# Kernel tuning notes

Measured on AMD Instinct MI355X. Metric: run time of the kernel, lower is better.

Reference implementation:

```python
import jax, jax.numpy as jnp
import numpy as np

N_HEAD = 16
LN_EPS = 1e-5


def _rope_tables(T, hd, dtype):
    # Standard GPT-NeoX style rotary tables: cos/sin of shape [T, hd]
    inv = 1.0 / (10000.0 ** (np.arange(0, hd, 2, dtype=np.float64) / hd))
    freqs = np.outer(np.arange(T), inv)
    emb = np.concatenate([freqs, freqs], axis=-1)
    return jnp.asarray(np.cos(emb), dtype), jnp.asarray(np.sin(emb), dtype)


def _rotate_half(x):
    x1, x2 = jnp.split(x, 2, axis=-1)
    return jnp.concatenate([-x2, x1], axis=-1)


def _layernorm(x, g, b):
    mu = x.mean(-1, keepdims=True)
    var = x.var(-1, keepdims=True)
    return (x - mu) / jnp.sqrt(var + LN_EPS) * g + b


def _heads(x, H):
    B, T, C = x.shape
    return x.reshape(B, T, H, C // H).transpose(0, 2, 1, 3)  # [B,H,T,hd]


def _lin_attention(Q, K, V, causal):
    # Q,K,V: [B,H,T,hd]; ELU+1 feature map, RoPE on features, denom = sum_s Q.K
    Qf = jax.nn.elu(Q) + 1.0
    Kf = jax.nn.elu(K) + 1.0
    hd = Qf.shape[-1]
    cq, sq = _rope_tables(Qf.shape[2], hd, Qf.dtype)
    ck, sk = _rope_tables(Kf.shape[2], hd, Kf.dtype)
    Qr = Qf * cq + _rotate_half(Qf) * sq
    Kr = Kf * ck + _rotate_half(Kf) * sk
    # denom.sum(-1) == Qf . (sum_s Kf) -- avoid materializing a second TxS matrix
    denom = jnp.einsum('bhtd,bhd->bht', Qf, Kf.sum(axis=2))[..., None]
    att = jnp.einsum('bhtd,bhsd->bhts', Qr, Kr)
    if causal:
        T, S = att.shape[-2], att.shape[-1]
        att = jnp.where(jnp.tril(jnp.ones((T, S), dtype=bool)), att, 0.0)
    att = att / denom
    y = jnp.einsum('bhts,bhsd->bhtd', att, V)
    B, H, T, hd = y.shape
    return y.transpose(0, 2, 1, 3).reshape(B, T, H * hd)


def _forward(x, memory, ln1_g, ln1_b, sa_qkv_w, sa_qkv_b, sa_proj_w, sa_proj_b,
             ln2_g, ln2_b, ca_q_w, ca_q_b, ca_kv_w, ca_kv_b, ca_proj_w, ca_proj_b,
             ln3_g, ln3_b, fc_w, fc_b, fcp_w, fcp_b):
    H = N_HEAD
    # causal self-attention
    h = _layernorm(x, ln1_g, ln1_b)
    qkv = h @ sa_qkv_w + sa_qkv_b
    Q, K, V = jnp.split(qkv, 3, axis=-1)
    y = _lin_attention(_heads(Q, H), _heads(K, H), _heads(V, H), causal=True)
    x = x + (y @ sa_proj_w + sa_proj_b)
    # cross-attention
    h = _layernorm(x, ln2_g, ln2_b)
    q = h @ ca_q_w + ca_q_b
    kv = memory @ ca_kv_w + ca_kv_b
    K, V = jnp.split(kv, 2, axis=-1)
    y = _lin_attention(_heads(q, H), _heads(K, H), _heads(V, H), causal=False)
    x = x + (y @ ca_proj_w + ca_proj_b)
    # MLP with tanh-approx GELU
    h = _layernorm(x, ln3_g, ln3_b)
    h = jax.nn.gelu(h @ fc_w + fc_b, approximate=True)
    x = x + (h @ fcp_w + fcp_b)
    return x


def setup_inputs() -> dict:
    key = jax.random.key(0)
    ks = jax.random.split(key, 12)
    B, T, S, C = 2, 1024, 1024, 1024
    w = lambda k, shape: jax.random.normal(k, shape, dtype=jnp.float32) * 0.02
    return {
        'x': jax.random.normal(ks[0], (B, T, C), dtype=jnp.float32),
        'memory': jax.random.normal(ks[1], (B, S, C), dtype=jnp.float32),
        'ln1_g': jnp.ones((C,), jnp.float32), 'ln1_b': jnp.zeros((C,), jnp.float32),
        'sa_qkv_w': w(ks[2], (C, 3 * C)), 'sa_qkv_b': jnp.zeros((3 * C,), jnp.float32),
        'sa_proj_w': w(ks[3], (C, C)), 'sa_proj_b': jnp.zeros((C,), jnp.float32),
        'ln2_g': jnp.ones((C,), jnp.float32), 'ln2_b': jnp.zeros((C,), jnp.float32),
        'ca_q_w': w(ks[4], (C, C)), 'ca_q_b': jnp.zeros((C,), jnp.float32),
        'ca_kv_w': w(ks[5], (C, 2 * C)), 'ca_kv_b': jnp.zeros((2 * C,), jnp.float32),
        'ca_proj_w': w(ks[6], (C, C)), 'ca_proj_b': jnp.zeros((C,), jnp.float32),
        'ln3_g': jnp.ones((C,), jnp.float32), 'ln3_b': jnp.zeros((C,), jnp.float32),
        'fc_w': w(ks[7], (C, 4 * C)), 'fc_b': jnp.zeros((4 * C,), jnp.float32),
        'fcp_w': w(ks[8], (4 * C, C)), 'fcp_b': jnp.zeros((C,), jnp.float32),
    }


def reference(x, memory, ln1_g, ln1_b, sa_qkv_w, sa_qkv_b, sa_proj_w, sa_proj_b,
              ln2_g, ln2_b, ca_q_w, ca_q_b, ca_kv_w, ca_kv_b, ca_proj_w, ca_proj_b,
              ln3_g, ln3_b, fc_w, fc_b, fcp_w, fcp_b):
    return _forward(x, memory, ln1_g, ln1_b, sa_qkv_w, sa_qkv_b, sa_proj_w, sa_proj_b,
                    ln2_g, ln2_b, ca_q_w, ca_q_b, ca_kv_w, ca_kv_b, ca_proj_w, ca_proj_b,
                    ln3_g, ln3_b, fc_w, fc_b, fcp_w, fcp_b)
```

## Files before the change

kernel.cpp:

```cpp
#include <hip/hip_runtime.h>
#include <math.h>

#define BB 2
#define TT 1024
#define CC 1024
#define HH 16
#define HD 64
#define MM (BB*TT)

typedef unsigned short u16;
typedef unsigned int u32;
typedef short s16x8 __attribute__((ext_vector_type(8)));
typedef float f32x4 __attribute__((ext_vector_type(4)));

__device__ __forceinline__ u16 f2bf(float f) {
    u32 u = __builtin_bit_cast(u32, f);
    u += 0x7fffu + ((u >> 16) & 1u);
    return (u16)(u >> 16);
}
__device__ __forceinline__ float bf2f(u16 h) {
    return __builtin_bit_cast(float, ((u32)h) << 16);
}
__device__ __forceinline__ void gload16(const void* g, void* l) {
    __builtin_amdgcn_global_load_lds((const __attribute__((address_space(1))) u32*)g,
                                     (__attribute__((address_space(3))) u32*)l, 16, 0, 0);
}
__device__ __forceinline__ float gelu_tanh(float x) {
    float x3 = x * x * x;
    return 0.5f * x * (1.0f + tanhf(0.7978845608028654f * (x + 0.044715f * x3)));
}
__device__ __forceinline__ float elu1(float v) {
    return (v > 0.0f) ? v + 1.0f : expf(v);
}

__device__ __forceinline__ void wtile(const float* __restrict__ in, u16* __restrict__ out,
                                      int K, int N, int local, float (*tl)[65]) {
    int tilesX = N >> 6;
    int n0 = (local % tilesX) * 64, k0 = (local / tilesX) * 64;
    int c = threadIdx.x & 63, r4 = threadIdx.x >> 6;
    #pragma unroll
    for (int i = 0; i < 16; ++i) {
        int r = r4 * 16 + i;
        tl[r][c] = in[(size_t)(k0 + r) * N + n0 + c];
    }
    __syncthreads();
    #pragma unroll
    for (int i = 0; i < 16; ++i) {
        int r = r4 * 16 + i;
        out[(size_t)(n0 + r) * K + k0 + c] = f2bf(tl[c][r]);
    }
}

__global__ __launch_bounds__(256) void prep_kernel(
        const float* __restrict__ w_qkv, u16* __restrict__ t_qkv,
        const float* __restrict__ w_pr,  u16* __restrict__ t_pr,
        const float* __restrict__ w_caq, u16* __restrict__ t_caq,
        const float* __restrict__ w_cakv,u16* __restrict__ t_cakv,
        const float* __restrict__ w_capr,u16* __restrict__ t_capr,
        const float* __restrict__ w_fc,  u16* __restrict__ t_fc,
        const float* __restrict__ w_fcp, u16* __restrict__ t_fcp,
        const float* __restrict__ memF,  u16* __restrict__ memB,
        float* __restrict__ cosT, float* __restrict__ sinT,
        const float* __restrict__ x, const float* __restrict__ ln1_g,
        const float* __restrict__ ln1_b, u16* __restrict__ hB) {
    __shared__ float tl[64][65];
    int bid = blockIdx.x;
    if (bid < 768)        wtile(w_qkv,  t_qkv,  1024, 3072, bid, tl);
    else if (bid < 1024)  wtile(w_pr,   t_pr,   1024, 1024, bid - 768, tl);
    else if (bid < 1280)  wtile(w_caq,  t_caq,  1024, 1024, bid - 1024, tl);
    else if (bid < 1792)  wtile(w_cakv, t_cakv, 1024, 2048, bid - 1280, tl);
    else if (bid < 2048)  wtile(w_capr, t_capr, 1024, 1024, bid - 1792, tl);
    else if (bid < 3072)  wtile(w_fc,   t_fc,   1024, 4096, bid - 2048, tl);
    else if (bid < 4096)  wtile(w_fcp,  t_fcp,  4096, 1024, bid - 3072, tl);
    else if (bid < 6144) {
        int i = (bid - 4096) * 256 + threadIdx.x;
        float4 v = reinterpret_cast<const float4*>(memF)[i];
        uint2 p;
        p.x = (u32)f2bf(v.x) | ((u32)f2bf(v.y) << 16);
        p.y = (u32)f2bf(v.z) | ((u32)f2bf(v.w) << 16);
        reinterpret_cast<uint2*>(memB)[i] = p;
    } else if (bid < 6272) {
        int idx = (bid - 6144) * 256 + threadIdx.x;
        int t = idx >> 5, d = idx & 31;
        double inv = pow(10000.0, -((double)d) / 32.0);
        double ang = (double)t * inv;
        cosT[t * 32 + d] = (float)cos(ang);
        sinT[t * 32 + d] = (float)sin(ang);
    } else {
        int row = bid - 6272;
        float4 v = reinterpret_cast<const float4*>(x + (size_t)row * CC)[threadIdx.x];
        float s  = v.x + v.y + v.z + v.w;
        float sq = v.x*v.x + v.y*v.y + v.z*v.z + v.w*v.w;
        #pragma unroll
        for (int off = 32; off >= 1; off >>= 1) {
            s  += __shfl_down(s, off);
            sq += __shfl_down(sq, off);
        }
        __shared__ float ls[4], lsq[4];
        int wave = threadIdx.x >> 6, lane = threadIdx.x & 63;
        if (lane == 0) { ls[wave] = s; lsq[wave] = sq; }
        __syncthreads();
        s  = ls[0] + ls[1] + ls[2] + ls[3];
        sq = lsq[0] + lsq[1] + lsq[2] + lsq[3];
        float mean = s * (1.0f / CC);
        float var  = sq * (1.0f / CC) - mean * mean;
        float rstd = rsqrtf(var + 1e-5f);
        float4 gv = reinterpret_cast<const float4*>(ln1_g)[threadIdx.x];
        float4 bv = reinterpret_cast<const float4*>(ln1_b)[threadIdx.x];
        float o0 = (v.x - mean) * rstd * gv.x + bv.x;
        float o1 = (v.y - mean) * rstd * gv.y + bv.y;
        float o2 = (v.z - mean) * rstd * gv.z + bv.z;
        float o3 = (v.w - mean) * rstd * gv.w + bv.w;
        uint2 p;
        p.x = (u32)f2bf(o0) | ((u32)f2bf(o1) << 16);
        p.y = (u32)f2bf(o2) | ((u32)f2bf(o3) << 16);
        reinterpret_cast<uint2*>(hB + (size_t)row * CC)[threadIdx.x] = p;
    }
}

#define M_F32RES 0
#define M_GELU   1
#define M_QKV    2
#define M_PART   5
#define M_CAQKV  6

template <int MODE>
__device__ __forceinline__ void emit(int row, int col, float v,
                                     const float* __restrict__ res,
                                     float* __restrict__ oF, u16* __restrict__ o1,
                                     u16* __restrict__ o2, u16* __restrict__ o3, int N) {
    if constexpr (MODE == M_F32RES) {
        size_t o = (size_t)row * N + col;
        oF[o] = v + res[o];
    } else if constexpr (MODE == M_GELU) {
        o1[(size_t)row * N + col] = f2bf(gelu_tanh(v));
    } else {
        int b = row >> 10, t = row & 1023;
        if (col < 1024) {
            int h = col >> 6, d = col & 63;
            o1[(((size_t)(b * HH + h)) * TT + t) * HD + d] = f2bf(elu1(v));
        } else if (col < 2048) {
            int c = col - 1024, h = c >> 6, d = c & 63;
            o2[(((size_t)(b * HH + h)) * TT + t) * HD + d] = f2bf(elu1(v));
        } else {
            int c = col - 2048, h = c >> 6, d = c & 63;
            o3[(((size_t)(b * HH + h)) * HD + d) * TT + t] = f2bf(v);
        }
    }
}

template <int BM, int BN, int MODE, int SPLITK>
__global__ __launch_bounds__(512, 8) void gemm_bf16(const u16* __restrict__ A,
                                                    const u16* __restrict__ A2,
                                                    const u16* __restrict__ BT,
                                                    const u16* __restrict__ BT2,
                                                    const float* __restrict__ bias,
                                                    const float* __restrict__ bias2,
                                                    const float* __restrict__ res,
                                                    float* __restrict__ oF,
                                                    u16* __restrict__ o1,
                                                    u16* __restrict__ o2,
                                                    u16* __restrict__ o3,
                                                    float* __restrict__ ksumP,
                                                    int N, int K) {
    constexpr int WM = BM / 4, WN = BN / 2;
    constexpr int FI = WM / 16, FJ = WN / 16;
    constexpr int IA = BM * 8 / 512;
    constexpr int IB = BN * 8 / 512;
    __shared__ u16 As[BM * 64];
    __shared__ u16 Bs[BN * 64];
    int tid = threadIdx.x;
    int wave = tid >> 6, lane = tid & 63;
    int wr = wave >> 1, wc = wave & 1;
    int gx = gridDim.x, gy = gridDim.y;
    int lid = blockIdx.x + gx * blockIdx.y;
    int chunk = (gx * gy) >> 3;
    int swz = (lid & 7) * chunk + (lid >> 3);
    int bx = swz % gx, by = swz / gx;
    int row0 = by * BM, col0 = bx * BN;
    const u16* Ause = A;
    const u16* Buse = BT;
    const float* buse = bias;
    if constexpr (MODE == M_CAQKV) {
        if (col0 >= 1024) {
            Ause = A2;
            Buse = BT2 - (size_t)1024 * K;
            buse = bias2 - 1024;
        }
    }
    int kbeg = 0, kcnt = K;
    if constexpr (SPLITK > 1) { kcnt = K / SPLITK; kbeg = blockIdx.z * kcnt; }
    int kend = kbeg + kcnt;

    f32x4 acc[FI][FJ] = {};
    int lr = lane & 15;
    for (int kt = kbeg; kt < kend; kt += 64) {
        __syncthreads();
        #pragma unroll
        for (int i = 0; i < IA; ++i) {
            int s = tid + i * 512;
            int r = s >> 3, kb = s & 7;
            int kbs = kb ^ (r & 7);
            gload16(Ause + (size_t)(row0 + r) * K + kt + kbs * 8, &As[s * 8]);
        }
        #pragma unroll
        for (int i = 0; i < IB; ++i) {
            int s = tid + i * 512;
            int r = s >> 3, kb = s & 7;
            int kbs = kb ^ (r & 7);
            gload16(Buse + (size_t)(col0 + r) * K + kt + kbs * 8, &Bs[s * 8]);
        }
        __syncthreads();
        #pragma unroll
        for (int ks = 0; ks < 2; ++ks) {
            s16x8 a[FI], b[FJ];
            int kc = ks * 4 + (lane >> 4);
            int sw = (kc ^ (lr & 7)) * 8;
            #pragma unroll
            for (int i = 0; i < FI; ++i)
                a[i] = *reinterpret_cast<const s16x8*>(&As[(wr * WM + i * 16 + lr) * 64 + sw]);
            #pragma unroll
            for (int j = 0; j < FJ; ++j)
                b[j] = *reinterpret_cast<const s16x8*>(&Bs[(wc * WN + j * 16 + lr) * 64 + sw]);
            __builtin_amdgcn_s_setprio(1);
            #pragma unroll
            for (int i = 0; i < FI; ++i)
                #pragma unroll
                for (int j = 0; j < FJ; ++j)
                    acc[i][j] = __builtin_amdgcn_mfma_f32_16x16x32_bf16(a[i], b[j], acc[i][j], 0, 0, 0);
            __builtin_amdgcn_s_setprio(0);
        }
    }
    int lr4 = (lane >> 4) * 4;
    if constexpr (MODE == M_PART) {
        size_t zoff = (size_t)blockIdx.z * (size_t)(gridDim.y * BM) * N;
        #pragma unroll
        for (int j = 0; j < FJ; ++j) {
            int col = col0 + wc * WN + j * 16 + lr;
            #pragma unroll
            for (int i = 0; i < FI; ++i)
                #pragma unroll
                for (int r = 0; r < 4; ++r) {
                    int row = row0 + wr * WM + i * 16 + lr4 + r;
                    oF[zoff + (size_t)row * N + col] = acc[i][j][r];
                }
        }
    } else {
        constexpr int EM = (MODE == M_CAQKV) ? M_QKV : MODE;
        #pragma unroll
        for (int j = 0; j < FJ; ++j) {
            int col = col0 + wc * WN + j * 16 + lr;
            float bi = buse[col];
            #pragma unroll
            for (int i = 0; i < FI; ++i)
                #pragma unroll
                for (int r = 0; r < 4; ++r) {
                    int row = row0 + wr * WM + i * 16 + lr4 + r;
                    emit<EM>(row, col, acc[i][j][r] + bi, res, oF, o1, o2, o3, N);
                }
        }
        if constexpr (MODE == M_QKV || MODE == M_CAQKV) {
            if (col0 >= 1024 && col0 < 2048) {
                float* scratch = (float*)As;
                float part[FJ];
                #pragma unroll
                for (int j = 0; j < FJ; ++j) {
                    int col = col0 + wc * WN + j * 16 + lr;
                    float bi = buse[col];
                    float p = 0.f;
                    #pragma unroll
                    for (int i = 0; i < FI; ++i)
                        #pragma unroll
                        for (int r = 0; r < 4; ++r)
                            p += elu1(acc[i][j][r] + bi);
                    part[j] = p;
                }
                __syncthreads();
                int contrib = wr * 4 + (lane >> 4);
                #pragma unroll
                for (int j = 0; j < FJ; ++j) {
                    int colLocal = wc * WN + j * 16 + lr;
                    scratch[colLocal * 16 + contrib] = part[j];
                }
                __syncthreads();
                if (tid < BN) {
                    float s = 0.f;
                    #pragma unroll
                    for (int c = 0; c < 16; ++c) s += scratch[tid * 16 + c];
                    ksumP[(size_t)by * 1024 + (col0 - 1024) + tid] = s;
                }
            }
        }
    }
}

template <int S>
__global__ __launch_bounds__(256) void reduce_res_kernel(const float* __restrict__ P,
                                                         const float* __restrict__ bias,
                                                         const float* __restrict__ res,
                                                         float* __restrict__ out,
                                                         int N, int total4) {
    int idx = blockIdx.x * 256 + threadIdx.x;
    if (idx >= total4) return;
    float4 b = reinterpret_cast<const float4*>(bias)[idx & (N / 4 - 1)];
    float4 r = reinterpret_cast<const float4*>(res)[idx];
    float4 a = {b.x + r.x, b.y + r.y, b.z + r.z, b.w + r.w};
    #pragma unroll
    for (int s = 0; s < S; ++s) {
        float4 p = reinterpret_cast<const float4*>(P)[(size_t)s * total4 + idx];
        a.x += p.x; a.y += p.y; a.z += p.z; a.w += p.w;
    }
    reinterpret_cast<float4*>(out)[idx] = a;
}

template <int S>
__global__ __launch_bounds__(256) void reduce_ln_kernel(const float* __restrict__ P,
                                                        const float* __restrict__ bias,
                                                        const float* __restrict__ res,
                                                        const float* __restrict__ g,
                                                        const float* __restrict__ bta,
                                                        float* __restrict__ out,
                                                        u16* __restrict__ hout) {
    int row = blockIdx.x;
    int t = threadIdx.x;
    const int total4 = MM * CC / 4;
    size_t ro4 = (size_t)row * 256 + t;
    float4 b = reinterpret_cast<const float4*>(bias)[t];
    float4 r = reinterpret_cast<const float4*>(res)[ro4];
    float4 a = {b.x + r.x, b.y + r.y, b.z + r.z, b.w + r.w};
    #pragma unroll
    for (int s = 0; s < S; ++s) {
        float4 p = reinterpret_cast<const float4*>(P)[(size_t)s * total4 + ro4];
        a.x += p.x; a.y += p.y; a.z += p.z; a.w += p.w;
    }
    reinterpret_cast<float4*>(out)[ro4] = a;
    float s1 = a.x + a.y + a.z + a.w;
    float sq = a.x*a.x + a.y*a.y + a.z*a.z + a.w*a.w;
    #pragma unroll
    for (int off = 32; off >= 1; off >>= 1) {
        s1 += __shfl_down(s1, off);
        sq += __shfl_down(sq, off);
    }
    __shared__ float ls[4], lsq[4];
    int wave = t >> 6, lane = t & 63;
    if (lane == 0) { ls[wave] = s1; lsq[wave] = sq; }
    __syncthreads();
    s1 = ls[0] + ls[1] + ls[2] + ls[3];
    sq = lsq[0] + lsq[1] + lsq[2] + lsq[3];
    float mean = s1 * (1.0f / CC);
    float var  = sq * (1.0f / CC) - mean * mean;
    float rstd = rsqrtf(var + 1e-5f);
    float4 gv = reinterpret_cast<const float4*>(g)[t];
    float4 bv = reinterpret_cast<const float4*>(bta)[t];
    float o0 = (a.x - mean) * rstd * gv.x + bv.x;
    float o1 = (a.y - mean) * rstd * gv.y + bv.y;
    float o2 = (a.z - mean) * rstd * gv.z + bv.z;
    float o3 = (a.w - mean) * rstd * gv.w + bv.w;
    uint2 pk;
    pk.x = (u32)f2bf(o0) | ((u32)f2bf(o1) << 16);
    pk.y = (u32)f2bf(o2) | ((u32)f2bf(o3) << 16);
    reinterpret_cast<uint2*>(hout + (size_t)row * CC)[t] = pk;
}

__device__ __forceinline__ void rope_row(u16* __restrict__ buf, int bh, int t, int q,
                                         const float* __restrict__ cosT,
                                         const float* __restrict__ sinT) {
    int d0 = q * 8;
    size_t base = ((size_t)bh * TT + t) * HD;
    s16x8 lo = *reinterpret_cast<const s16x8*>(&buf[base + d0]);
    s16x8 hi = *reinterpret_cast<const s16x8*>(&buf[base + 32 + d0]);
    const float4* cp = reinterpret_cast<const float4*>(&cosT[t * 32 + d0]);
    const float4* sp = reinterpret_cast<const float4*>(&sinT[t * 32 + d0]);
    float4 c0 = cp[0], c1 = cp[1], s0 = sp[0], s1 = sp[1];
    float cc[8] = {c0.x, c0.y, c0.z, c0.w, c1.x, c1.y, c1.z, c1.w};
    float ss[8] = {s0.x, s0.y, s0.z, s0.w, s1.x, s1.y, s1.z, s1.w};
    s16x8 nlo, nhi;
    #pragma unroll
    for (int e = 0; e < 8; ++e) {
        float l = bf2f((u16)lo[e]), h = bf2f((u16)hi[e]);
        nlo[e] = (short)f2bf(l * cc[e] - h * ss[e]);
        nhi[e] = (short)f2bf(h * cc[e] + l * ss[e]);
    }
    *reinterpret_cast<s16x8*>(&buf[base + d0]) = nlo;
    *reinterpret_cast<s16x8*>(&buf[base + 32 + d0]) = nhi;
}

__global__ __launch_bounds__(256) void denom_rope_kernel(u16* __restrict__ Qb,
                                                         u16* __restrict__ Kb,
                                                         const float* __restrict__ KsumP,
                                                         const float* __restrict__ cosT,
                                                         const float* __restrict__ sinT,
                                                         float* __restrict__ den) {
    int bid = blockIdx.x;
    if (bid < 1024) {
        int bh = bid >> 5;
        int b = bh >> 4, h = bh & 15;
        int t0 = (bid & 31) * 32;
        __shared__ float ks[64];
        if (threadIdx.x < 64) {
            float s = 0.f;
            #pragma unroll
            for (int rb = 0; rb < 8; ++rb)
                s += KsumP[(size_t)(b * 8 + rb) * 1024 + h * 64 + threadIdx.x];
            ks[threadIdx.x] = s;
        }
        __syncthreads();
        int wave = threadIdx.x >> 6, lane = threadIdx.x & 63;
        int rw = lane >> 3, lsub = lane & 7;
        int t = t0 + wave * 8 + rw;
        s16x8 q = *reinterpret_cast<const s16x8*>(&Qb[((size_t)bh * TT + t) * HD + lsub * 8]);
        float p = 0.f;
        #pragma unroll
        for (int e = 0; e < 8; ++e) p += bf2f((u16)q[e]) * ks[lsub * 8 + e];
        p += __shfl_xor(p, 1);
        p += __shfl_xor(p, 2);
        p += __shfl_xor(p, 4);
        if (lsub == 0) den[bh * TT + t] = p;
        __syncthreads();
        if (threadIdx.x < 128) {
            int row = threadIdx.x >> 2, qq = threadIdx.x & 3;
            rope_row(Qb, bh, t0 + row, qq, cosT, sinT);
        }
    } else {
        int g = (bid - 1024) * 256 + threadIdx.x;
        int qq = g & 3;
        int t = (g >> 2) & 1023;
        int bh = g >> 12;
        rope_row(Kb, bh, t, qq, cosT, sinT);
    }
}

#define APAD 72
__global__ __launch_bounds__(256) void attn_mfma(const u16* __restrict__ Qr,
                                                 const u16* __restrict__ Kr,
                                                 const u16* __restrict__ VT,
                                                 const float* __restrict__ den,
                                                 u16* __restrict__ out, int causal) {
    __shared__ u16 Qs[64 * APAD];
    __shared__ u16 Ks[64 * APAD];
    __shared__ u16 Vs[64 * APAD];
    __shared__ u16 Ps[64 * APAD];
    int lid = blockIdx.x + gridDim.x * blockIdx.y;
    int chunk = (gridDim.x * gridDim.y) >> 3;
    int swz = (lid & 7) * chunk + (lid >> 3);
    int tile = swz % gridDim.x;
    int bh = swz / gridDim.x;
    int b = bh >> 4, h = bh & 15;
    int t0 = tile * 64;
    int tid = threadIdx.x, wave = tid >> 6, lane = tid & 63;
    #pragma unroll
    for (int i = 0; i < 2; ++i) {
        int s = tid + i * 256;
        int r = s >> 3, kb = s & 7;
        *reinterpret_cast<s16x8*>(&Qs[r * APAD + kb * 8]) =
            *reinterpret_cast<const s16x8*>(&Qr[((size_t)bh * TT + t0 + r) * HD + kb * 8]);
    }
    __syncthreads();
    int lr = lane & 15, lk = (lane >> 4) * 8;
    s16x8 qf0 = *reinterpret_cast<const s16x8*>(&Qs[(wave * 16 + lr) * APAD + lk]);
    s16x8 qf1 = *reinterpret_cast<const s16x8*>(&Qs[(wave * 16 + lr) * APAD + 32 + lk]);
    f32x4 accO[4] = {};
    int ntiles = causal ? (tile + 1) : (TT / 64);
    for (int st = 0; st < ntiles; ++st) {
        int s0 = st * 64;
        __syncthreads();
        #pragma unroll
        for (int i = 0; i < 2; ++i) {
            int s = tid + i * 256;
            int r = s >> 3, kb = s & 7;
            *reinterpret_cast<s16x8*>(&Ks[r * APAD + kb * 8]) =
                *reinterpret_cast<const s16x8*>(&Kr[((size_t)bh * TT + s0 + r) * HD + kb * 8]);
            *reinterpret_cast<s16x8*>(&Vs[r * APAD + kb * 8]) =
                *reinterpret_cast<const s16x8*>(&VT[((size_t)bh * HD + r) * TT + s0 + kb * 8]);
        }
        __syncthreads();
        f32x4 accS[4] = {};
        __builtin_amdgcn_s_setprio(1);
        #pragma unroll
        for (int j = 0; j < 4; ++j) {
            s16x8 kb0 = *reinterpret_cast<const s16x8*>(&Ks[(j * 16 + lr) * APAD + lk]);
            s16x8 kb1 = *reinterpret_cast<const s16x8*>(&Ks[(j * 16 + lr) * APAD + 32 + lk]);
            accS[j] = __builtin_amdgcn_mfma_f32_16x16x32_bf16(qf0, kb0, accS[j], 0, 0, 0);
            accS[j] = __builtin_amdgcn_mfma_f32_16x16x32_bf16(qf1, kb1, accS[j], 0, 0, 0);
        }
        __builtin_amdgcn_s_setprio(0);
        int tl = wave * 16 + (lane >> 4) * 4;
        #pragma unroll
        for (int j = 0; j < 4; ++j) {
            #pragma unroll
            for (int r = 0; r < 4; ++r) {
                float v = accS[j][r];
                if (causal && (s0 + j * 16 + lr > t0 + tl + r)) v = 0.f;
                Ps[(tl + r) * APAD + j * 16 + lr] = f2bf(v);
            }
        }
        __syncthreads();
        __builtin_amdgcn_s_setprio(1);
        #pragma unroll
        for (int ks = 0; ks < 2; ++ks) {
            s16x8 pa = *reinterpret_cast<const s16x8*>(&Ps[(wave * 16 + lr) * APAD + ks * 32 + lk]);
            #pragma unroll
            for (int j = 0; j < 4; ++j) {
                s16x8 vb = *reinterpret_cast<const s16x8*>(&Vs[(j * 16 + lr) * APAD + ks * 32 + lk]);
                accO[j] = __builtin_amdgcn_mfma_f32_16x16x32_bf16(pa, vb, accO[j], 0, 0, 0);
            }
        }
        __builtin_amdgcn_s_setprio(0);
    }
    int tl = wave * 16 + (lane >> 4) * 4;
    float invd[4];
    #pragma unroll
    for (int r = 0; r < 4; ++r) invd[r] = 1.0f / den[bh * TT + t0 + tl + r];
    #pragma unroll
    for (int j = 0; j < 4; ++j)
        #pragma unroll
        for (int r = 0; r < 4; ++r)
            out[(size_t)(b * TT + t0 + tl + r) * CC + h * HD + j * 16 + lr] = f2bf(accO[j][r] * invd[r]);
}

extern "C" void kernel_launch(void* const* d_in, const int* in_sizes, int n_in,
                              void* d_out, int out_size, void* d_ws, size_t ws_size,
                              hipStream_t stream) {
    const float* x        = (const float*)d_in[0];
    const float* memory   = (const float*)d_in[1];
    const float* ln1_g    = (const float*)d_in[2];
    const float* ln1_b    = (const float*)d_in[3];
    const float* sa_qkv_w = (const float*)d_in[4];
    const float* sa_qkv_b = (const float*)d_in[5];
    const float* sa_pr_w  = (const float*)d_in[6];
    const float* sa_pr_b  = (const float*)d_in[7];
    const float* ln2_g    = (const float*)d_in[8];
    const float* ln2_b    = (const float*)d_in[9];
    const float* ca_q_w   = (const float*)d_in[10];
    const float* ca_q_b   = (const float*)d_in[11];
    const float* ca_kv_w  = (const float*)d_in[12];
    const float* ca_kv_b  = (const float*)d_in[13];
    const float* ca_pr_w  = (const float*)d_in[14];
    const float* ca_pr_b  = (const float*)d_in[15];
    const float* ln3_g    = (const float*)d_in[16];
    const float* ln3_b    = (const float*)d_in[17];
    const float* fc_w     = (const float*)d_in[18];
    const float* fc_b     = (const float*)d_in[19];
    const float* fcp_w    = (const float*)d_in[20];
    const float* fcp_b    = (const float*)d_in[21];
    float* out = (float*)d_out;
    char* wsb  = (char*)d_ws;

    const size_t MB = 1024 * 1024;
    u16* qkvT  = (u16*)wsb;
    u16* prT   = (u16*)(wsb + 6 * MB);
    u16* caqT  = (u16*)(wsb + 8 * MB);
    u16* cakvT = (u16*)(wsb + 10 * MB);
    u16* caprT = (u16*)(wsb + 14 * MB);
    u16* fcT   = (u16*)(wsb + 16 * MB);
    u16* fcpT  = (u16*)(wsb + 24 * MB);
    u16* memB  = (u16*)(wsb + 32 * MB);
    u16* hB    = (u16*)(wsb + 36 * MB);
    u16* h2B   = (u16*)(wsb + 40 * MB);
    u16* Qb    = (u16*)(wsb + 44 * MB);
    u16* Kb    = (u16*)(wsb + 48 * MB);
    u16* VTb   = (u16*)(wsb + 52 * MB);
    float* Pbuf = (float*)(wsb + 44 * MB);
    u16* fcB   = (u16*)(wsb + 60 * MB);
    float* KsumP = (float*)(wsb + 76 * MB + 65536);
    float* den   = (float*)(wsb + 76 * MB + 131072);
    float* cosT  = (float*)(wsb + 76 * MB + 262144);
    float* sinT  = (float*)(wsb + 76 * MB + 393216);

    dim3 b256(256), b512(512);
    const int TOT4 = MM * CC / 4;

    prep_kernel<<<dim3(8320), b256, 0, stream>>>(
        sa_qkv_w, qkvT, sa_pr_w, prT, ca_q_w, caqT, ca_kv_w, cakvT,
        ca_pr_w, caprT, fc_w, fcT, fcp_w, fcpT, memory, memB, cosT, sinT,
        x, ln1_g, ln1_b, hB);

    gemm_bf16<128, 64, M_QKV, 1><<<dim3(48, 16), b512, 0, stream>>>(
        hB, nullptr, qkvT, nullptr, sa_qkv_b, nullptr, nullptr,
        nullptr, Qb, Kb, VTb, KsumP, 3072, 1024);
    denom_rope_kernel<<<dim3(1536), b256, 0, stream>>>(Qb, Kb, KsumP, cosT, sinT, den);
    attn_mfma<<<dim3(16, 32), b256, 0, stream>>>(Qb, Kb, VTb, den, h2B, 1);
    gemm_bf16<64, 64, M_PART, 2><<<dim3(16, 32, 2), b512, 0, stream>>>(
        h2B, nullptr, prT, nullptr, nullptr, nullptr, nullptr,
        Pbuf, nullptr, nullptr, nullptr, nullptr, 1024, 1024);
    reduce_ln_kernel<2><<<dim3(MM), b256, 0, stream>>>(Pbuf, sa_pr_b, x, ln2_g, ln2_b, out, hB);

    gemm_bf16<128, 64, M_CAQKV, 1><<<dim3(48, 16), b512, 0, stream>>>(
        hB, memB, caqT, cakvT, ca_q_b, ca_kv_b, nullptr,
        nullptr, Qb, Kb, VTb, KsumP, 3072, 1024);
    denom_rope_kernel<<<dim3(1536), b256, 0, stream>>>(Qb, Kb, KsumP, cosT, sinT, den);
    attn_mfma<<<dim3(16, 32), b256, 0, stream>>>(Qb, Kb, VTb, den, h2B, 0);
    gemm_bf16<64, 64, M_PART, 2><<<dim3(16, 32, 2), b512, 0, stream>>>(
        h2B, nullptr, caprT, nullptr, nullptr, nullptr, nullptr,
        Pbuf, nullptr, nullptr, nullptr, nullptr, 1024, 1024);
    reduce_ln_kernel<2><<<dim3(MM), b256, 0, stream>>>(Pbuf, ca_pr_b, out, ln3_g, ln3_b, out, hB);

    gemm_bf16<128, 64, M_GELU, 1><<<dim3(64, 16), b512, 0, stream>>>(
        hB, nullptr, fcT, nullptr, fc_b, nullptr, nullptr,
        nullptr, fcB, nullptr, nullptr, nullptr, 4096, 1024);
    gemm_bf16<128, 64, M_PART, 2><<<dim3(16, 16, 2), b512, 0, stream>>>(
        fcB, nullptr, fcpT, nullptr, nullptr, nullptr, nullptr,
        Pbuf, nullptr, nullptr, nullptr, nullptr, 1024, 4096);
    reduce_res_kernel<2><<<dim3(TOT4 / 256), b256, 0, stream>>>(Pbuf, fcp_b, out, out, 1024, TOT4);
}
```

Measured before the change: 232.3 us.

## Double-buffer GEMM LDS tiles to overlap global loads with MFMA

Splits the GEMM shared-memory tiles into two buffers and issues the global-to-LDS loads for the next K tile before computing on the current one. Explicit vmcnt waits and raw s_barriers replace the two __syncthreads per iteration, so load latency can hide behind MFMA work. This doubles LDS use per block, which may lower occupancy under the 512-thread launch bounds. Correctness depends on the hand-written waitcnt counts matching the number of outstanding loads.

```diff
diff --git a/kernel.cpp b/kernel.cpp
--- a/kernel.cpp
+++ b/kernel.cpp
@@ -24,6 +24,16 @@
 __device__ __forceinline__ void gload16(const void* g, void* l) {
     __builtin_amdgcn_global_load_lds((const __attribute__((address_space(1))) u32*)g,
                                      (__attribute__((address_space(3))) u32*)l, 16, 0, 0);
+}
+template <int N> __device__ __forceinline__ void vmwait() {
+    static_assert(N >= 0 && N <= 6, "");
+    if constexpr (N == 0) asm volatile("s_waitcnt vmcnt(0)" ::: "memory");
+    else if constexpr (N == 1) asm volatile("s_waitcnt vmcnt(1)" ::: "memory");
+    else if constexpr (N == 2) asm volatile("s_waitcnt vmcnt(2)" ::: "memory");
+    else if constexpr (N == 3) asm volatile("s_waitcnt vmcnt(3)" ::: "memory");
+    else if constexpr (N == 4) asm volatile("s_waitcnt vmcnt(4)" ::: "memory");
+    else if constexpr (N == 5) asm volatile("s_waitcnt vmcnt(5)" ::: "memory");
+    else asm volatile("s_waitcnt vmcnt(6)" ::: "memory");
 }
 __device__ __forceinline__ float gelu_tanh(float x) {
     float x3 = x * x * x;
@@ -167,8 +177,9 @@
     constexpr int FI = WM / 16, FJ = WN / 16;
     constexpr int IA = BM * 8 / 512;
     constexpr int IB = BN * 8 / 512;
-    __shared__ u16 As[BM * 64];
-    __shared__ u16 Bs[BN * 64];
+    constexpr int NL = IA + IB;
+    __shared__ u16 As[2][BM * 64];
+    __shared__ u16 Bs[2][BN * 64];
     int tid = threadIdx.x;
     int wave = tid >> 6, lane = tid & 63;
     int wr = wave >> 1, wc = wave & 1;
@@ -192,25 +203,36 @@
     if constexpr (SPLITK > 1) { kcnt = K / SPLITK; kbeg = blockIdx.z * kcnt; }
     int kend = kbeg + kcnt;
 
-    f32x4 acc[FI][FJ] = {};
-    int lr = lane & 15;
-    for (int kt = kbeg; kt < kend; kt += 64) {
-        __syncthreads();
+    auto stage = [&](int buf, int kt) {
         #pragma unroll
         for (int i = 0; i < IA; ++i) {
             int s = tid + i * 512;
             int r = s >> 3, kb = s & 7;
             int kbs = kb ^ (r & 7);
-            gload16(Ause + (size_t)(row0 + r) * K + kt + kbs * 8, &As[s * 8]);
+            gload16(Ause + (size_t)(row0 + r) * K + kt + kbs * 8, &As[buf][s * 8]);
         }
         #pragma unroll
         for (int i = 0; i < IB; ++i) {
             int s = tid + i * 512;
             int r = s >> 3, kb = s & 7;
             int kbs = kb ^ (r & 7);
-            gload16(Buse + (size_t)(col0 + r) * K + kt + kbs * 8, &Bs[s * 8]);
-        }
-        __syncthreads();
+            gload16(Buse + (size_t)(col0 + r) * K + kt + kbs * 8, &Bs[buf][s * 8]);
+        }
+    };
+
+    f32x4 acc[FI][FJ] = {};
+    int lr = lane & 15;
+    stage(0, kbeg);
+    int cur = 0;
+    for (int kt = kbeg; kt < kend; kt += 64) {
+        if (kt + 64 < kend) {
+            stage(cur ^ 1, kt + 64);
+            vmwait<NL>();
+        } else {
+            vmwait<0>();
+        }
+        __builtin_amdgcn_s_barrier();
+        __builtin_amdgcn_sched_barrier(0);
         #pragma unroll
         for (int ks = 0; ks < 2; ++ks) {
             s16x8 a[FI], b[FJ];
@@ -218,10 +240,10 @@
             int sw = (kc ^ (lr & 7)) * 8;
             #pragma unroll
             for (int i = 0; i < FI; ++i)
-                a[i] = *reinterpret_cast<const s16x8*>(&As[(wr * WM + i * 16 + lr) * 64 + sw]);
+                a[i] = *reinterpret_cast<const s16x8*>(&As[cur][(wr * WM + i * 16 + lr) * 64 + sw]);
             #pragma unroll
             for (int j = 0; j < FJ; ++j)
-                b[j] = *reinterpret_cast<const s16x8*>(&Bs[(wc * WN + j * 16 + lr) * 64 + sw]);
+                b[j] = *reinterpret_cast<const s16x8*>(&Bs[cur][(wc * WN + j * 16 + lr) * 64 + sw]);
             __builtin_amdgcn_s_setprio(1);
             #pragma unroll
             for (int i = 0; i < FI; ++i)
@@ -230,6 +252,9 @@
                     acc[i][j] = __builtin_amdgcn_mfma_f32_16x16x32_bf16(a[i], b[j], acc[i][j], 0, 0, 0);
             __builtin_amdgcn_s_setprio(0);
         }
+        __builtin_amdgcn_sched_barrier(0);
+        __builtin_amdgcn_s_barrier();
+        cur ^= 1;
     }
     int lr4 = (lane >> 4) * 4;
     if constexpr (MODE == M_PART) {
```

After: 236.5 us. About the same (+1.8%).
